# Kernel tuning notes

Hardware: AMD Instinct MI355X
Metric: run time of the kernel (lower is better)

Reference implementation:

```python
import jax, jax.numpy as jnp
import numpy as np

STATE_DIM = 32
ACTION_DIM = 8
LATENT_DIM = 64
HIDDEN = 128
X_DIM = ACTION_DIM + 1  # t channel + actions
B = 4096
L = 128
N_SUB = 2  # fixed RK4 substeps per knot interval


def natural_cubic_coeffs(x):
    """Natural cubic spline on unit-spaced knots 0..L-1 (matches torchcde's
    implicit arange grid). x: [B, L, C]. Returns per-interval coeffs b, c, d
    ([B, L-1, C]) s.t. X(i+u) = x_i + b u + c u^2 + d u^3."""
    Bb, Ln, C = x.shape
    n = Ln - 2
    # tridiagonal system for interior second derivatives (natural BC: m0=mL-1=0)
    M = 4.0 * jnp.eye(n, dtype=x.dtype) + jnp.eye(n, k=1, dtype=x.dtype) + jnp.eye(n, k=-1, dtype=x.dtype)
    rhs = 6.0 * (x[:, 2:] - 2.0 * x[:, 1:-1] + x[:, :-2])  # [B, n, C]
    m_in = jnp.linalg.solve(M, rhs.transpose(1, 0, 2).reshape(n, -1))  # [n, B*C]
    m_in = m_in.reshape(n, Bb, C).transpose(1, 0, 2)
    zpad = jnp.zeros((Bb, 1, C), x.dtype)
    m = jnp.concatenate([zpad, m_in, zpad], axis=1)  # [B, L, C]
    b = (x[:, 1:] - x[:, :-1]) - (2.0 * m[:, :-1] + m[:, 1:]) / 6.0
    c = m[:, :-1] / 2.0
    d = (m[:, 1:] - m[:, :-1]) / 6.0
    return b, c, d


def setup_inputs() -> dict:
    key = jax.random.key(0)
    ks = jax.random.split(key, 8)
    s = jax.random.normal(ks[0], (B, L, STATE_DIM), dtype=jnp.float32)
    a = jax.random.normal(ks[1], (B, L, ACTION_DIM), dtype=jnp.float32)
    t = jnp.broadcast_to(jnp.arange(L, dtype=jnp.float32), (B, L)) + jnp.zeros((B, L), jnp.float32)

    def lin(k, fi, fo, scale=1.0):
        return (jax.random.normal(k, (fi, fo), dtype=jnp.float32) * (scale / np.sqrt(fi))).astype(jnp.float32)

    enc_W = lin(ks[2], STATE_DIM + ACTION_DIM + 1, LATENT_DIM)
    enc_b = jnp.zeros((LATENT_DIM,), jnp.float32)
    f_W1 = lin(ks[3], LATENT_DIM, HIDDEN, 0.5)
    f_b1 = jnp.zeros((HIDDEN,), jnp.float32)
    f_W2 = lin(ks[4], HIDDEN, LATENT_DIM * X_DIM, 0.1)  # small scale keeps the CDE stable over 127 time units
    f_b2 = jnp.zeros((LATENT_DIM * X_DIM,), jnp.float32)
    dec_W = lin(ks[5], LATENT_DIM, STATE_DIM)
    dec_b = jnp.zeros((STATE_DIM,), jnp.float32)
    return dict(s=s, a=a, t=t, enc_W=enc_W, enc_b=enc_b, f_W1=f_W1, f_b1=f_b1,
                f_W2=f_W2, f_b2=f_b2, dec_W=dec_W, dec_b=dec_b)


def reference(s, a, t, enc_W, enc_b, f_W1, f_b1, f_W2, f_b2, dec_W, dec_b):
    # control path X = [t, a] : [B, L, X_DIM]
    x = jnp.concatenate([t[..., None], a], axis=-1)
    cb, cc, cd = natural_cubic_coeffs(x)  # each [B, L-1, X_DIM]

    z0 = jnp.concatenate([s[:, 0], a[:, 0], t[:, 0:1]], axis=-1) @ enc_W + enc_b  # [B, latent]

    def vf(z):  # f(z): [B, latent] -> [B, latent, X_DIM]
        h = jax.nn.relu(z @ f_W1 + f_b1)
        return (h @ f_W2 + f_b2).reshape(-1, LATENT_DIM, X_DIM)

    hstep = 1.0 / N_SUB

    def interval(z, coef):
        bi, ci, di = coef  # [B, X_DIM] each, current interval spline coeffs

        def dzdu(z, u):
            dX = bi + 2.0 * ci * u + 3.0 * di * (u * u)  # dX/dt on this interval
            return jnp.einsum('blx,bx->bl', vf(z), dX)

        for k in range(N_SUB):  # small fixed unroll, not a data-dim loop
            u = k * hstep
            k1 = dzdu(z, u)
            k2 = dzdu(z + 0.5 * hstep * k1, u + 0.5 * hstep)
            k3 = dzdu(z + 0.5 * hstep * k2, u + 0.5 * hstep)
            k4 = dzdu(z + hstep * k3, u + hstep)
            z = z + (hstep / 6.0) * (k1 + 2.0 * k2 + 2.0 * k3 + k4)
        return z, z

    coefs = (cb.transpose(1, 0, 2), cc.transpose(1, 0, 2), cd.transpose(1, 0, 2))  # [L-1, B, X_DIM]
    _, zs = jax.lax.scan(interval, z0, coefs)  # zs: [L-1, B, latent]
    z = jnp.concatenate([z0[None], zs], axis=0).transpose(1, 0, 2)  # [B, L, latent]
    return z @ dec_W + dec_b  # [B, L, state_dim]
```

## Files before the change

kernel.cpp:

```cpp
#include <hip/hip_runtime.h>

#define Bsz 4096
#define Lsz 128
#define NI  127
#define SD  32
#define AD  8
#define LAT 64
#define HID 128
#define BT  16
#define THR 1024

typedef float f32x2 __attribute__((ext_vector_type(2)));
typedef float f32x4 __attribute__((ext_vector_type(4)));

__global__ __launch_bounds__(256) void repack_w2(const float* __restrict__ W2,
                                                 float* __restrict__ W2p8,
                                                 float* __restrict__ W2c0){
  int idx = blockIdx.x*256 + threadIdx.x;
  if (idx < HID*LAT*8){
    int x = idx & 7; int jl = idx >> 3; int l = jl & 63; int j = jl >> 6;
    W2p8[idx] = W2[(j*LAT + l)*9 + x + 1];
  } else if (idx < HID*LAT*9){
    int jl = idx - HID*LAT*8;
    W2c0[jl] = W2[(size_t)jl*9];
  }
}

__global__ __launch_bounds__(256) void spline_kernel(const float* __restrict__ a,
                                                     float* __restrict__ m_ws){
  __shared__ float cp_s[126];
  if (threadIdx.x == 0){
    float c = 0.25f; cp_s[0] = c;
    for (int i=1;i<126;i++){ c = 1.0f/(4.0f - c); cp_s[i] = c; }
  }
  __syncthreads();
  int tid = blockIdx.x*256 + threadIdx.x;
  int b = tid >> 3, c8 = tid & 7;
  float dp[126];
  const float* ab = a + (size_t)b*Lsz*AD + c8;
  float x0 = ab[0];
  float x1 = ab[AD];
  for (int i=0;i<126;i++){
    float x2 = ab[(size_t)(i+2)*AD];
    float rhs = 6.0f*(x2 - 2.0f*x1 + x0);
    dp[i] = (i==0)? rhs*0.25f : (rhs - dp[i-1])*cp_s[i];
    x0 = x1; x1 = x2;
  }
  m_ws[tid] = 0.0f;
  m_ws[((size_t)127*Bsz)*8 + tid] = 0.0f;
  float mn = 0.0f;
  for (int k=125;k>=0;k--){
    mn = dp[k] - cp_s[k]*mn;
    m_ws[((size_t)(k+1)*Bsz)*8 + tid] = mn;
  }
}

#define DPP_XOR1(v) __int_as_float(__builtin_amdgcn_mov_dpp(__float_as_int(v), 0xB1, 0xF, 0xF, true))
#define DPP_XOR2(v) __int_as_float(__builtin_amdgcn_mov_dpp(__float_as_int(v), 0x4E, 0xF, 0xF, true))
#define SWZ_XOR4(v) __int_as_float(__builtin_amdgcn_ds_swizzle(__float_as_int(v), 0x101F))
#define SWZ_XOR8(v) __int_as_float(__builtin_amdgcn_ds_swizzle(__float_as_int(v), 0x201F))

#define PK_MUL_BCLO(d, w, x) asm("v_pk_mul_f32 %0, %1, %2 op_sel:[0,0] op_sel_hi:[0,1]" : "=v"(d) : "v"(w), "v"(x))
#define PK_FMA_BCLO(acc, w, x) asm("v_pk_fma_f32 %0, %1, %2, %0 op_sel:[0,0,0] op_sel_hi:[0,1,1]" : "+v"(acc) : "v"(w), "v"(x))
#define PK_FMA_BCHI(acc, w, x) asm("v_pk_fma_f32 %0, %1, %2, %0 op_sel:[1,0,0] op_sel_hi:[1,1,1]" : "+v"(acc) : "v"(w), "v"(x))
#define PK_FMA(acc, a, b)      asm("v_pk_fma_f32 %0, %1, %2, %0" : "+v"(acc) : "v"(a), "v"(b))
#define PK_ADD(d, a, b)        asm("v_pk_add_f32 %0, %1, %2" : "=v"(d) : "v"(a), "v"(b))

#define LO2(v4) __builtin_shufflevector(v4, v4, 0, 1)
#define HI2(v4) __builtin_shufflevector(v4, v4, 2, 3)

#define HPROW 324
#define DXROW 20

__attribute__((amdgpu_waves_per_eu(4,4)))
__global__ __launch_bounds__(THR) void cde_integrate(
    const float* __restrict__ s, const float* __restrict__ a, const float* __restrict__ t,
    const float* __restrict__ encW, const float* __restrict__ encb,
    const float* __restrict__ W1, const float* __restrict__ b1,
    const float* __restrict__ b2, const float* __restrict__ decW, const float* __restrict__ decb,
    const float* __restrict__ W2p8, const float* __restrict__ W2c0, const float* __restrict__ m_ws,
    float* __restrict__ out)
{
  __shared__ float W1t[HID][LAT+4];
  __shared__ float hp[8*HPROW];
  __shared__ float zs[BT][LAT+4];
  __shared__ float dXp[5*160];
  __shared__ float dWs[LAT][SD];
  __shared__ float b1s[HID];
  __shared__ float b2s[LAT][12];
  __shared__ float dbs[SD];

  const int tid = threadIdx.x;
  const int b0 = blockIdx.x * BT;

  for (int i=tid;i<HID*LAT;i+=THR){ int j = i & (HID-1); int k = i >> 7; W1t[j][k] = W1[k*HID+j]; }
  for (int i=tid;i<LAT*SD;i+=THR)  ((float*)dWs)[i] = decW[i];
  if (tid < HID) b1s[tid] = b1[tid];
  for (int i=tid;i<LAT*12;i+=THR){ int l=i/12, x=i%12; b2s[l][x] = (x<9)? b2[l*9+x] : 0.f; }
  if (tid < SD) dbs[tid] = decb[tid];

  const int ol = tid >> 4;
  const int jg = tid & 15;

  f32x2 wpk[8][4]; f32x2 wc0pk[4];
  {
    #pragma unroll
    for (int jj=0;jj<8;jj++){
      const f32x2* p2 = (const f32x2*)&W2p8[((size_t)(jg*8+jj)*LAT + ol)*8];
      wpk[jj][0]=p2[0]; wpk[jj][1]=p2[1]; wpk[jj][2]=p2[2]; wpk[jj][3]=p2[3];
    }
    #pragma unroll
    for (int q=0;q<4;q++){
      wc0pk[q].x = W2c0[(jg*8+2*q)*LAT + ol];
      wc0pk[q].y = W2c0[(jg*8+2*q+1)*LAT + ol];
    }
  }
  const f32x2 one11 = {1.0f, 1.0f};

  {
    const int bb = tid >> 6;
    const int li = tid & 63;
    const float* sb = s + (size_t)(b0+bb)*Lsz*SD;
    const float* ab = a + (size_t)(b0+bb)*Lsz*AD;
    const float tv = t[(size_t)(b0+bb)*Lsz];
    float acc = encb[li];
    #pragma unroll
    for (int k=0;k<SD;k++) acc = fmaf(sb[k], encW[k*LAT+li], acc);
    #pragma unroll
    for (int k=0;k<AD;k++) acc = fmaf(ab[k], encW[(SD+k)*LAT+li], acc);
    acc = fmaf(tv, encW[(SD+AD)*LAT+li], acc);
    zs[bb][li] = acc;
  }
  __syncthreads();

  if (tid < BT*SD){
    const int bb = tid >> 5; const int o = tid & 31;
    float acc = dbs[o];
    #pragma unroll 8
    for (int k=0;k<LAT;k++) acc = fmaf(zs[bb][k], dWs[k][o], acc);
    out[((size_t)(b0+bb)*Lsz + 0)*SD + o] = acc;
  }

  float zb = zs[jg][ol];
  float ka = 0.f;

  const int hwaddr = (jg>>1)*HPROW + (ol>>2)*20 + ((2*ol)&7)*2 + (jg&1);

  for (int iv=0; iv<NI; iv++){
    if (tid < 5*BT*8){
      int ui = tid >> 7; int r = tid & 127; int bb = r >> 3; int x8 = r & 7;
      float u = 0.25f*(float)ui;
      int gb = b0+bb;
      float m0 = m_ws[((size_t)iv    *Bsz + gb)*8 + x8];
      float m1 = m_ws[((size_t)(iv+1)*Bsz + gb)*8 + x8];
      float xd = a[((size_t)gb*Lsz + iv+1)*AD + x8] - a[((size_t)gb*Lsz + iv)*AD + x8];
      float cb = xd - (2.f*m0 + m1)*(1.f/6.f);
      float cc = 0.5f*m0;
      float cd = (m1 - m0)*(1.f/6.f);
      dXp[ui*160 + (bb>>1)*DXROW + x8*2 + (bb&1)] = cb + (2.f*cc)*u + (3.f*cd)*(u*u);
    }

    for (int st=0; st<8; st++){
      const int ui = (st+1)>>1;
      const int mode = st & 3;
      __syncthreads();

      {
        const int j0 = 2*ol;
        float acc0 = b1s[j0], acc1 = b1s[j0+1];
        const float4* z4 = (const float4*)&zs[jg][0];
        const float4* w0 = (const float4*)&W1t[j0][0];
        const float4* w1 = (const float4*)&W1t[j0+1][0];
        #pragma unroll
        for (int k4=0;k4<LAT/4;k4++){
          float4 zv = z4[k4]; float4 u0 = w0[k4]; float4 u1 = w1[k4];
          acc0 = fmaf(zv.x,u0.x,acc0); acc0 = fmaf(zv.y,u0.y,acc0);
          acc0 = fmaf(zv.z,u0.z,acc0); acc0 = fmaf(zv.w,u0.w,acc0);
          acc1 = fmaf(zv.x,u1.x,acc1); acc1 = fmaf(zv.y,u1.y,acc1);
          acc1 = fmaf(zv.z,u1.z,acc1); acc1 = fmaf(zv.w,u1.w,acc1);
        }
        hp[hwaddr]   = fmaxf(acc0, 0.f);
        hp[hwaddr+2] = fmaxf(acc1, 0.f);
      }
      __syncthreads();

      f32x2 tot0, tot1;
      #pragma unroll
      for (int bbat=0; bbat<2; bbat++){
        f32x2 dzp[4];
        #pragma unroll
        for (int i=0;i<4;i++){ dzp[i].x = 0.f; dzp[i].y = 0.f; }
        #pragma unroll
        for (int pi=0; pi<4; pi++){
          const int p = bbat*4 + pi;
          const f32x4* dxq = (const f32x4*)&dXp[ui*160 + p*DXROW];
          const f32x4* hq  = (const f32x4*)&hp[p*HPROW + jg*20];
          f32x4 d0=dxq[0], d1=dxq[1], d2=dxq[2], d3=dxq[3];
          f32x4 g0=hq[0],  g1=hq[1],  g2=hq[2],  g3=hq[3];
          f32x2 dx2[8] = {LO2(d0),HI2(d0),LO2(d1),HI2(d1),LO2(d2),HI2(d2),LO2(d3),HI2(d3)};
          f32x2 hh [8] = {LO2(g0),HI2(g0),LO2(g1),HI2(g1),LO2(g2),HI2(g2),LO2(g3),HI2(g3)};
          #pragma unroll
          for (int jj=0;jj<8;jj++){
            f32x2 wd;
            PK_MUL_BCLO(wd, wpk[jj][0], dx2[0]);
            PK_FMA_BCHI(wd, wpk[jj][0], dx2[1]);
            PK_FMA_BCLO(wd, wpk[jj][1], dx2[2]);
            PK_FMA_BCHI(wd, wpk[jj][1], dx2[3]);
            PK_FMA_BCLO(wd, wpk[jj][2], dx2[4]);
            PK_FMA_BCHI(wd, wpk[jj][2], dx2[5]);
            PK_FMA_BCLO(wd, wpk[jj][3], dx2[6]);
            PK_FMA_BCHI(wd, wpk[jj][3], dx2[7]);
            if ((jj&1)==0){ PK_FMA_BCLO(wd, wc0pk[jj>>1], one11); }
            else          { PK_FMA_BCHI(wd, wc0pk[jj>>1], one11); }
            PK_FMA(dzp[pi], hh[jj], wd);
          }
        }
        const bool g1 = (jg>>1)&1;
        f32x2 nd[2];
        #pragma unroll
        for (int i=0;i<2;i++){
          f32x2 lo = dzp[2*i], hi = dzp[2*i+1];
          f32x2 send = g1 ? lo : hi;
          f32x2 recv; recv.x = DPP_XOR2(send.x); recv.y = DPP_XOR2(send.y);
          f32x2 keep = g1 ? hi : lo;
          PK_ADD(nd[i], keep, recv);
        }
        const bool g2 = (jg>>2)&1;
        f32x2 md;
        {
          f32x2 lo = nd[0], hi = nd[1];
          f32x2 send = g2 ? lo : hi;
          f32x2 recv; recv.x = SWZ_XOR4(send.x); recv.y = SWZ_XOR4(send.y);
          f32x2 keep = g2 ? hi : lo;
          PK_ADD(md, keep, recv);
        }
        f32x2 r8; r8.x = SWZ_XOR8(md.x); r8.y = SWZ_XOR8(md.y);
        f32x2 totv; PK_ADD(totv, md, r8);
        if (bbat==0) tot0 = totv; else tot1 = totv;
      }
      f32x2 sel = (jg&8) ? tot1 : tot0;
      float own = (jg&1) ? sel.y : sel.x;
      float oth = (jg&1) ? sel.x : sel.y;
      float dzm = own + DPP_XOR1(oth);

      {
        const f32x4* dxb = (const f32x4*)&dXp[ui*160 + (jg>>1)*DXROW];
        f32x4 q0=dxb[0], q1=dxb[1], q2=dxb[2], q3=dxb[3];
        const bool hi = (jg&1);
        float d0 = hi? q0.y:q0.x, d1 = hi? q0.w:q0.z;
        float d2 = hi? q1.y:q1.x, d3 = hi? q1.w:q1.z;
        float d4 = hi? q2.y:q2.x, d5 = hi? q2.w:q2.z;
        float d6 = hi? q3.y:q3.x, d7 = hi? q3.w:q3.z;
        const float4 ba = *(const float4*)&b2s[ol][0];
        const float4 bb4 = *(const float4*)&b2s[ol][4];
        float bias = fmaf(ba.y,d0, fmaf(ba.z,d1, fmaf(ba.w,d2, fmaf(bb4.x,d3,
                     fmaf(bb4.y,d4, fmaf(bb4.z,d5, fmaf(bb4.w,d6, fmaf(b2s[ol][8],d7, ba.x))))))));
        dzm += bias;
      }

      if (mode == 0){        ka = dzm;
        zs[jg][ol] = zb + 0.25f*dzm;
      } else if (mode == 1){ ka = fmaf(2.f, dzm, ka);
        zs[jg][ol] = zb + 0.25f*dzm;
      } else if (mode == 2){ ka = fmaf(2.f, dzm, ka);
        zs[jg][ol] = zb + 0.5f*dzm;
      } else {               ka += dzm;
        zb = fmaf(0.5f/6.f, ka, zb);
        zs[jg][ol] = zb;
      }
    }

    __syncthreads();
    if (tid < BT*SD){
      const int bb = tid >> 5; const int o = tid & 31;
      float acc = dbs[o];
      #pragma unroll 8
      for (int k=0;k<LAT;k++) acc = fmaf(zs[bb][k], dWs[k][o], acc);
      out[((size_t)(b0+bb)*Lsz + (iv+1))*SD + o] = acc;
    }
  }
}

extern "C" void kernel_launch(void* const* d_in, const int* in_sizes, int n_in,
                              void* d_out, int out_size, void* d_ws, size_t ws_size,
                              hipStream_t stream){
  const float* s    = (const float*)d_in[0];
  const float* a    = (const float*)d_in[1];
  const float* t    = (const float*)d_in[2];
  const float* encW = (const float*)d_in[3];
  const float* encb = (const float*)d_in[4];
  const float* W1   = (const float*)d_in[5];
  const float* b1   = (const float*)d_in[6];
  const float* W2   = (const float*)d_in[7];
  const float* b2   = (const float*)d_in[8];
  const float* decW = (const float*)d_in[9];
  const float* decb = (const float*)d_in[10];
  float* out = (float*)d_out;
  float* ws  = (float*)d_ws;
  float* W2p8 = ws;
  float* W2c0 = ws + HID*LAT*8;
  float* m_ws = ws + HID*LAT*9;

  hipLaunchKernelGGL(repack_w2, dim3((HID*LAT*9+255)/256), dim3(256), 0, stream, W2, W2p8, W2c0);
  hipLaunchKernelGGL(spline_kernel, dim3(Bsz*8/256), dim3(256), 0, stream, a, m_ws);
  hipLaunchKernelGGL(cde_integrate, dim3(Bsz/BT), dim3(THR), 0, stream,
                     s,a,t,encW,encb,W1,b1,b2,decW,decb,W2p8,W2c0,m_ws,out);
}
```

Before: 8.841 ms.

## Halve block threads, give each thread 16 hidden units and two batch rows

Cuts the block to 512 threads with 2 waves per EU. Each thread now keeps twice as many W2 weights in registers (16 hidden units) and computes two batch elements packed with v_pk instructions. The layer-1 matmul, the bias and the state update are all done with packed FMAs on interleaved z pairs, and the b1/b2 biases move from LDS into registers. The cross-lane reduction shrinks to an 8-lane xor tree. This aims to cut LDS traffic and reduction overhead per FLOP, at the cost of much higher register pressure and lower occupancy.

```diff
diff --git a/kernel.cpp b/kernel.cpp
--- a/kernel.cpp
+++ b/kernel.cpp
@@ -8,7 +8,7 @@
 #define LAT 64
 #define HID 128
 #define BT  16
-#define THR 1024
+#define THR 512
 
 typedef float f32x2 __attribute__((ext_vector_type(2)));
 typedef float f32x4 __attribute__((ext_vector_type(4)));
@@ -58,9 +58,9 @@
 #define DPP_XOR1(v) __int_as_float(__builtin_amdgcn_mov_dpp(__float_as_int(v), 0xB1, 0xF, 0xF, true))
 #define DPP_XOR2(v) __int_as_float(__builtin_amdgcn_mov_dpp(__float_as_int(v), 0x4E, 0xF, 0xF, true))
 #define SWZ_XOR4(v) __int_as_float(__builtin_amdgcn_ds_swizzle(__float_as_int(v), 0x101F))
-#define SWZ_XOR8(v) __int_as_float(__builtin_amdgcn_ds_swizzle(__float_as_int(v), 0x201F))
 
 #define PK_MUL_BCLO(d, w, x) asm("v_pk_mul_f32 %0, %1, %2 op_sel:[0,0] op_sel_hi:[0,1]" : "=v"(d) : "v"(w), "v"(x))
+#define PK_MUL_BCHI(d, w, x) asm("v_pk_mul_f32 %0, %1, %2 op_sel:[1,0] op_sel_hi:[1,1]" : "=v"(d) : "v"(w), "v"(x))
 #define PK_FMA_BCLO(acc, w, x) asm("v_pk_fma_f32 %0, %1, %2, %0 op_sel:[0,0,0] op_sel_hi:[0,1,1]" : "+v"(acc) : "v"(w), "v"(x))
 #define PK_FMA_BCHI(acc, w, x) asm("v_pk_fma_f32 %0, %1, %2, %0 op_sel:[1,0,0] op_sel_hi:[1,1,1]" : "+v"(acc) : "v"(w), "v"(x))
 #define PK_FMA(acc, a, b)      asm("v_pk_fma_f32 %0, %1, %2, %0" : "+v"(acc) : "v"(a), "v"(b))
@@ -69,10 +69,7 @@
 #define LO2(v4) __builtin_shufflevector(v4, v4, 0, 1)
 #define HI2(v4) __builtin_shufflevector(v4, v4, 2, 3)
 
-#define HPROW 324
-#define DXROW 20
-
-__attribute__((amdgpu_waves_per_eu(4,4)))
+__attribute__((amdgpu_waves_per_eu(2,2)))
 __global__ __launch_bounds__(THR) void cde_integrate(
     const float* __restrict__ s, const float* __restrict__ a, const float* __restrict__ t,
     const float* __restrict__ encW, const float* __restrict__ encb,
@@ -82,73 +79,85 @@
     float* __restrict__ out)
 {
   __shared__ float W1t[HID][LAT+4];
-  __shared__ float hp[8*HPROW];
-  __shared__ float zs[BT][LAT+4];
-  __shared__ float dXp[5*160];
+  __shared__ float hp[8][292];
+  __shared__ float zp[8][132];
+  __shared__ float dXp[5][8][20];
   __shared__ float dWs[LAT][SD];
-  __shared__ float b1s[HID];
-  __shared__ float b2s[LAT][12];
   __shared__ float dbs[SD];
 
   const int tid = threadIdx.x;
   const int b0 = blockIdx.x * BT;
+  const int ol = tid >> 3;
+  const int jg = tid & 7;
 
   for (int i=tid;i<HID*LAT;i+=THR){ int j = i & (HID-1); int k = i >> 7; W1t[j][k] = W1[k*HID+j]; }
   for (int i=tid;i<LAT*SD;i+=THR)  ((float*)dWs)[i] = decW[i];
-  if (tid < HID) b1s[tid] = b1[tid];
-  for (int i=tid;i<LAT*12;i+=THR){ int l=i/12, x=i%12; b2s[l][x] = (x<9)? b2[l*9+x] : 0.f; }
   if (tid < SD) dbs[tid] = decb[tid];
 
-  const int ol = tid >> 4;
-  const int jg = tid & 15;
-
-  f32x2 wpk[8][4]; f32x2 wc0pk[4];
+  f32x2 wpk[16][4]; f32x2 wc0pk[8];
   {
     #pragma unroll
-    for (int jj=0;jj<8;jj++){
-      const f32x2* p2 = (const f32x2*)&W2p8[((size_t)(jg*8+jj)*LAT + ol)*8];
+    for (int jj=0;jj<16;jj++){
+      const f32x2* p2 = (const f32x2*)&W2p8[((size_t)(jg*16+jj)*LAT + ol)*8];
       wpk[jj][0]=p2[0]; wpk[jj][1]=p2[1]; wpk[jj][2]=p2[2]; wpk[jj][3]=p2[3];
     }
     #pragma unroll
-    for (int q=0;q<4;q++){
-      wc0pk[q].x = W2c0[(jg*8+2*q)*LAT + ol];
-      wc0pk[q].y = W2c0[(jg*8+2*q+1)*LAT + ol];
-    }
-  }
-  const f32x2 one11 = {1.0f, 1.0f};
-
+    for (int q=0;q<8;q++){
+      wc0pk[q].x = W2c0[(jg*16+2*q)*LAT + ol];
+      wc0pk[q].y = W2c0[(jg*16+2*q+1)*LAT + ol];
+    }
+    #pragma unroll
+    for (int jj=0;jj<16;jj++){
+      asm volatile("" : "+v"(wpk[jj][0]), "+v"(wpk[jj][1]), "+v"(wpk[jj][2]), "+v"(wpk[jj][3]));
+    }
+  }
+  f32x2 b2p[4]; f32x2 b2c0v; f32x2 b1pair; f32x2 one11; one11.x = 1.f; one11.y = 1.f;
   {
-    const int bb = tid >> 6;
+    const float* bp = b2 + ol*9;
+    b2c0v.x = bp[0]; b2c0v.y = 0.f;
+    b2p[0].x = bp[1]; b2p[0].y = bp[2];
+    b2p[1].x = bp[3]; b2p[1].y = bp[4];
+    b2p[2].x = bp[5]; b2p[2].y = bp[6];
+    b2p[3].x = bp[7]; b2p[3].y = bp[8];
+    b1pair.x = b1[2*ol]; b1pair.y = b1[2*ol+1];
+  }
+
+  {
+    const int bb8 = tid >> 6;
     const int li = tid & 63;
-    const float* sb = s + (size_t)(b0+bb)*Lsz*SD;
-    const float* ab = a + (size_t)(b0+bb)*Lsz*AD;
-    const float tv = t[(size_t)(b0+bb)*Lsz];
-    float acc = encb[li];
     #pragma unroll
-    for (int k=0;k<SD;k++) acc = fmaf(sb[k], encW[k*LAT+li], acc);
-    #pragma unroll
-    for (int k=0;k<AD;k++) acc = fmaf(ab[k], encW[(SD+k)*LAT+li], acc);
-    acc = fmaf(tv, encW[(SD+AD)*LAT+li], acc);
-    zs[bb][li] = acc;
+    for (int h=0; h<2; h++){
+      const int b = bb8 + 8*h;
+      const float* sb = s + (size_t)(b0+b)*Lsz*SD;
+      const float* ab = a + (size_t)(b0+b)*Lsz*AD;
+      const float tv = t[(size_t)(b0+b)*Lsz];
+      float acc = encb[li];
+      #pragma unroll
+      for (int k=0;k<SD;k++) acc = fmaf(sb[k], encW[k*LAT+li], acc);
+      #pragma unroll
+      for (int k=0;k<AD;k++) acc = fmaf(ab[k], encW[(SD+k)*LAT+li], acc);
+      acc = fmaf(tv, encW[(SD+AD)*LAT+li], acc);
+      zp[b>>1][li*2 + (b&1)] = acc;
+    }
   }
   __syncthreads();
 
-  if (tid < BT*SD){
-    const int bb = tid >> 5; const int o = tid & 31;
+  {
+    const int bb = tid >> 5; const int o = tid & 31; const int c = bb & 1;
+    const float* zrow = &zp[bb>>1][0];
     float acc = dbs[o];
-    #pragma unroll 8
-    for (int k=0;k<LAT;k++) acc = fmaf(zs[bb][k], dWs[k][o], acc);
+    #pragma unroll 16
+    for (int k=0;k<LAT;k++) acc = fmaf(zrow[2*k+c], dWs[k][o], acc);
     out[((size_t)(b0+bb)*Lsz + 0)*SD + o] = acc;
   }
 
-  float zb = zs[jg][ol];
-  float ka = 0.f;
-
-  const int hwaddr = (jg>>1)*HPROW + (ol>>2)*20 + ((2*ol)&7)*2 + (jg&1);
-
+  float zb0, zb1, ka0 = 0.f, ka1 = 0.f;
+  { f32x2 zr = *(const f32x2*)&zp[jg][2*ol]; zb0 = zr.x; zb1 = zr.y; }
+
+  #pragma unroll 1
   for (int iv=0; iv<NI; iv++){
-    if (tid < 5*BT*8){
-      int ui = tid >> 7; int r = tid & 127; int bb = r >> 3; int x8 = r & 7;
+    for (int idx=tid; idx<5*BT*8; idx+=THR){
+      int ui = idx >> 7; int r = idx & 127; int bb = r >> 3; int x8 = r & 7;
       float u = 0.25f*(float)ui;
       int gb = b0+bb;
       float m0 = m_ws[((size_t)iv    *Bsz + gb)*8 + x8];
@@ -157,9 +166,10 @@
       float cb = xd - (2.f*m0 + m1)*(1.f/6.f);
       float cc = 0.5f*m0;
       float cd = (m1 - m0)*(1.f/6.f);
-      dXp[ui*160 + (bb>>1)*DXROW + x8*2 + (bb&1)] = cb + (2.f*cc)*u + (3.f*cd)*(u*u);
-    }
-
+      dXp[ui][bb>>1][x8*2 + (bb&1)] = cb + (2.f*cc)*u + (3.f*cd)*(u*u);
+    }
+
+    #pragma unroll 1
     for (int st=0; st<8; st++){
       const int ui = (st+1)>>1;
       const int mode = st & 3;
@@ -167,115 +177,133 @@
 
       {
         const int j0 = 2*ol;
-        float acc0 = b1s[j0], acc1 = b1s[j0+1];
-        const float4* z4 = (const float4*)&zs[jg][0];
-        const float4* w0 = (const float4*)&W1t[j0][0];
-        const float4* w1 = (const float4*)&W1t[j0+1][0];
+        f32x2 acc0, acc1;
+        PK_MUL_BCLO(acc0, b1pair, one11);
+        PK_MUL_BCHI(acc1, b1pair, one11);
+        const f32x4* zrow = (const f32x4*)&zp[jg][0];
+        const f32x4* w0r = (const f32x4*)&W1t[j0][0];
+        const f32x4* w1r = (const f32x4*)&W1t[j0+1][0];
         #pragma unroll
-        for (int k4=0;k4<LAT/4;k4++){
-          float4 zv = z4[k4]; float4 u0 = w0[k4]; float4 u1 = w1[k4];
-          acc0 = fmaf(zv.x,u0.x,acc0); acc0 = fmaf(zv.y,u0.y,acc0);
-          acc0 = fmaf(zv.z,u0.z,acc0); acc0 = fmaf(zv.w,u0.w,acc0);
-          acc1 = fmaf(zv.x,u1.x,acc1); acc1 = fmaf(zv.y,u1.y,acc1);
-          acc1 = fmaf(zv.z,u1.z,acc1); acc1 = fmaf(zv.w,u1.w,acc1);
+        for (int k16=0;k16<16;k16++){
+          f32x4 zqA = zrow[2*k16], zqB = zrow[2*k16+1];
+          f32x4 w0q = w0r[k16], w1q = w1r[k16];
+          f32x2 w0l = LO2(w0q), w0h = HI2(w0q), w1l = LO2(w1q), w1h = HI2(w1q);
+          f32x2 zA0 = LO2(zqA), zA1 = HI2(zqA), zB0 = LO2(zqB), zB1 = HI2(zqB);
+          PK_FMA_BCLO(acc0, w0l, zA0); PK_FMA_BCHI(acc0, w0l, zA1);
+          PK_FMA_BCLO(acc0, w0h, zB0); PK_FMA_BCHI(acc0, w0h, zB1);
+          PK_FMA_BCLO(acc1, w1l, zA0); PK_FMA_BCHI(acc1, w1l, zA1);
+          PK_FMA_BCLO(acc1, w1h, zB0); PK_FMA_BCHI(acc1, w1h, zB1);
         }
-        hp[hwaddr]   = fmaxf(acc0, 0.f);
-        hp[hwaddr+2] = fmaxf(acc1, 0.f);
+        f32x4 hv;
+        hv.x = fmaxf(acc0.x, 0.f); hv.y = fmaxf(acc0.y, 0.f);
+        hv.z = fmaxf(acc1.x, 0.f); hv.w = fmaxf(acc1.y, 0.f);
+        *(f32x4*)&hp[jg][(ol>>3)*36 + (ol&7)*4] = hv;
       }
       __syncthreads();
 
-      f32x2 tot0, tot1;
-      #pragma unroll
-      for (int bbat=0; bbat<2; bbat++){
-        f32x2 dzp[4];
+      f32x2 dz[8];
+      #pragma unroll
+      for (int p=0;p<8;p++){
+        const f32x4* dxr = (const f32x4*)&dXp[ui][p][0];
+        f32x4 d0=dxr[0], d1=dxr[1], d2=dxr[2], d3=dxr[3];
+        f32x2 dx2[8] = {LO2(d0),HI2(d0),LO2(d1),HI2(d1),LO2(d2),HI2(d2),LO2(d3),HI2(d3)};
+        const f32x4* hr = (const f32x4*)&hp[p][jg*36];
+        f32x2 acc; acc.x = 0.f; acc.y = 0.f;
         #pragma unroll
-        for (int i=0;i<4;i++){ dzp[i].x = 0.f; dzp[i].y = 0.f; }
-        #pragma unroll
-        for (int pi=0; pi<4; pi++){
-          const int p = bbat*4 + pi;
-          const f32x4* dxq = (const f32x4*)&dXp[ui*160 + p*DXROW];
-          const f32x4* hq  = (const f32x4*)&hp[p*HPROW + jg*20];
-          f32x4 d0=dxq[0], d1=dxq[1], d2=dxq[2], d3=dxq[3];
-          f32x4 g0=hq[0],  g1=hq[1],  g2=hq[2],  g3=hq[3];
-          f32x2 dx2[8] = {LO2(d0),HI2(d0),LO2(d1),HI2(d1),LO2(d2),HI2(d2),LO2(d3),HI2(d3)};
-          f32x2 hh [8] = {LO2(g0),HI2(g0),LO2(g1),HI2(g1),LO2(g2),HI2(g2),LO2(g3),HI2(g3)};
-          #pragma unroll
-          for (int jj=0;jj<8;jj++){
+        for (int jj2=0;jj2<8;jj2++){
+          f32x4 hq = hr[jj2];
+          f32x2 hl = LO2(hq), hh = HI2(hq);
+          {
             f32x2 wd;
-            PK_MUL_BCLO(wd, wpk[jj][0], dx2[0]);
-            PK_FMA_BCHI(wd, wpk[jj][0], dx2[1]);
-            PK_FMA_BCLO(wd, wpk[jj][1], dx2[2]);
-            PK_FMA_BCHI(wd, wpk[jj][1], dx2[3]);
-            PK_FMA_BCLO(wd, wpk[jj][2], dx2[4]);
-            PK_FMA_BCHI(wd, wpk[jj][2], dx2[5]);
-            PK_FMA_BCLO(wd, wpk[jj][3], dx2[6]);
-            PK_FMA_BCHI(wd, wpk[jj][3], dx2[7]);
-            if ((jj&1)==0){ PK_FMA_BCLO(wd, wc0pk[jj>>1], one11); }
-            else          { PK_FMA_BCHI(wd, wc0pk[jj>>1], one11); }
-            PK_FMA(dzp[pi], hh[jj], wd);
+            PK_MUL_BCLO(wd, wpk[2*jj2][0], dx2[0]); PK_FMA_BCHI(wd, wpk[2*jj2][0], dx2[1]);
+            PK_FMA_BCLO(wd, wpk[2*jj2][1], dx2[2]); PK_FMA_BCHI(wd, wpk[2*jj2][1], dx2[3]);
+            PK_FMA_BCLO(wd, wpk[2*jj2][2], dx2[4]); PK_FMA_BCHI(wd, wpk[2*jj2][2], dx2[5]);
+            PK_FMA_BCLO(wd, wpk[2*jj2][3], dx2[6]); PK_FMA_BCHI(wd, wpk[2*jj2][3], dx2[7]);
+            PK_FMA_BCLO(wd, wc0pk[jj2], one11);
+            PK_FMA(acc, hl, wd);
+          }
+          {
+            f32x2 wd;
+            PK_MUL_BCLO(wd, wpk[2*jj2+1][0], dx2[0]); PK_FMA_BCHI(wd, wpk[2*jj2+1][0], dx2[1]);
+            PK_FMA_BCLO(wd, wpk[2*jj2+1][1], dx2[2]); PK_FMA_BCHI(wd, wpk[2*jj2+1][1], dx2[3]);
+            PK_FMA_BCLO(wd, wpk[2*jj2+1][2], dx2[4]); PK_FMA_BCHI(wd, wpk[2*jj2+1][2], dx2[5]);
+            PK_FMA_BCLO(wd, wpk[2*jj2+1][3], dx2[6]); PK_FMA_BCHI(wd, wpk[2*jj2+1][3], dx2[7]);
+            PK_FMA_BCHI(wd, wc0pk[jj2], one11);
+            PK_FMA(acc, hh, wd);
           }
         }
-        const bool g1 = (jg>>1)&1;
-        f32x2 nd[2];
-        #pragma unroll
-        for (int i=0;i<2;i++){
-          f32x2 lo = dzp[2*i], hi = dzp[2*i+1];
-          f32x2 send = g1 ? lo : hi;
-          f32x2 recv; recv.x = DPP_XOR2(send.x); recv.y = DPP_XOR2(send.y);
-          f32x2 keep = g1 ? hi : lo;
-          PK_ADD(nd[i], keep, recv);
-        }
-        const bool g2 = (jg>>2)&1;
-        f32x2 md;
-        {
-          f32x2 lo = nd[0], hi = nd[1];
-          f32x2 send = g2 ? lo : hi;
-          f32x2 recv; recv.x = SWZ_XOR4(send.x); recv.y = SWZ_XOR4(send.y);
-          f32x2 keep = g2 ? hi : lo;
-          PK_ADD(md, keep, recv);
-        }
-        f32x2 r8; r8.x = SWZ_XOR8(md.x); r8.y = SWZ_XOR8(md.y);
-        f32x2 totv; PK_ADD(totv, md, r8);
-        if (bbat==0) tot0 = totv; else tot1 = totv;
-      }
-      f32x2 sel = (jg&8) ? tot1 : tot0;
-      float own = (jg&1) ? sel.y : sel.x;
-      float oth = (jg&1) ? sel.x : sel.y;
-      float dzm = own + DPP_XOR1(oth);
-
+        dz[p] = acc;
+      }
+
+      const bool g1 = jg & 1;
+      f32x2 n4[4];
+      #pragma unroll
+      for (int i=0;i<4;i++){
+        f32x2 lo = dz[2*i], hi = dz[2*i+1];
+        f32x2 send = g1 ? lo : hi;
+        f32x2 recv; recv.x = DPP_XOR1(send.x); recv.y = DPP_XOR1(send.y);
+        f32x2 keep = g1 ? hi : lo;
+        PK_ADD(n4[i], keep, recv);
+      }
+      const bool g2 = jg & 2;
+      f32x2 n2[2];
+      #pragma unroll
+      for (int i=0;i<2;i++){
+        f32x2 lo = n4[2*i], hi = n4[2*i+1];
+        f32x2 send = g2 ? lo : hi;
+        f32x2 recv; recv.x = DPP_XOR2(send.x); recv.y = DPP_XOR2(send.y);
+        f32x2 keep = g2 ? hi : lo;
+        PK_ADD(n2[i], keep, recv);
+      }
+      const bool g4 = jg & 4;
+      f32x2 res;
       {
-        const f32x4* dxb = (const f32x4*)&dXp[ui*160 + (jg>>1)*DXROW];
-        f32x4 q0=dxb[0], q1=dxb[1], q2=dxb[2], q3=dxb[3];
-        const bool hi = (jg&1);
-        float d0 = hi? q0.y:q0.x, d1 = hi? q0.w:q0.z;
-        float d2 = hi? q1.y:q1.x, d3 = hi? q1.w:q1.z;
-        float d4 = hi? q2.y:q2.x, d5 = hi? q2.w:q2.z;
-        float d6 = hi? q3.y:q3.x, d7 = hi? q3.w:q3.z;
-        const float4 ba = *(const float4*)&b2s[ol][0];
-        const float4 bb4 = *(const float4*)&b2s[ol][4];
-        float bias = fmaf(ba.y,d0, fmaf(ba.z,d1, fmaf(ba.w,d2, fmaf(bb4.x,d3,
-                     fmaf(bb4.y,d4, fmaf(bb4.z,d5, fmaf(bb4.w,d6, fmaf(b2s[ol][8],d7, ba.x))))))));
-        dzm += bias;
-      }
-
-      if (mode == 0){        ka = dzm;
-        zs[jg][ol] = zb + 0.25f*dzm;
-      } else if (mode == 1){ ka = fmaf(2.f, dzm, ka);
-        zs[jg][ol] = zb + 0.25f*dzm;
-      } else if (mode == 2){ ka = fmaf(2.f, dzm, ka);
-        zs[jg][ol] = zb + 0.5f*dzm;
-      } else {               ka += dzm;
-        zb = fmaf(0.5f/6.f, ka, zb);
-        zs[jg][ol] = zb;
-      }
+        f32x2 lo = n2[0], hi = n2[1];
+        f32x2 send = g4 ? lo : hi;
+        f32x2 recv; recv.x = SWZ_XOR4(send.x); recv.y = SWZ_XOR4(send.y);
+        f32x2 keep = g4 ? hi : lo;
+        PK_ADD(res, keep, recv);
+      }
+
+      f32x2 bias2;
+      {
+        const f32x4* dxb = (const f32x4*)&dXp[ui][jg][0];
+        f32x4 e0=dxb[0], e1=dxb[1], e2=dxb[2], e3=dxb[3];
+        PK_MUL_BCLO(bias2, b2c0v, one11);
+        PK_FMA_BCLO(bias2, b2p[0], LO2(e0)); PK_FMA_BCHI(bias2, b2p[0], HI2(e0));
+        PK_FMA_BCLO(bias2, b2p[1], LO2(e1)); PK_FMA_BCHI(bias2, b2p[1], HI2(e1));
+        PK_FMA_BCLO(bias2, b2p[2], LO2(e2)); PK_FMA_BCHI(bias2, b2p[2], HI2(e2));
+        PK_FMA_BCLO(bias2, b2p[3], LO2(e3)); PK_FMA_BCHI(bias2, b2p[3], HI2(e3));
+      }
+      f32x2 dzm2; PK_ADD(dzm2, res, bias2);
+      const float dz0 = dzm2.x, dz1 = dzm2.y;
+
+      float zn0, zn1;
+      if (mode == 0){
+        ka0 = dz0; ka1 = dz1;
+        zn0 = fmaf(0.25f, dz0, zb0); zn1 = fmaf(0.25f, dz1, zb1);
+      } else if (mode == 1){
+        ka0 = fmaf(2.f, dz0, ka0); ka1 = fmaf(2.f, dz1, ka1);
+        zn0 = fmaf(0.25f, dz0, zb0); zn1 = fmaf(0.25f, dz1, zb1);
+      } else if (mode == 2){
+        ka0 = fmaf(2.f, dz0, ka0); ka1 = fmaf(2.f, dz1, ka1);
+        zn0 = fmaf(0.5f, dz0, zb0); zn1 = fmaf(0.5f, dz1, zb1);
+      } else {
+        ka0 += dz0; ka1 += dz1;
+        zb0 = fmaf(0.5f/6.f, ka0, zb0); zb1 = fmaf(0.5f/6.f, ka1, zb1);
+        zn0 = zb0; zn1 = zb1;
+      }
+      f32x2 zw; zw.x = zn0; zw.y = zn1;
+      *(f32x2*)&zp[jg][2*ol] = zw;
     }
 
     __syncthreads();
-    if (tid < BT*SD){
-      const int bb = tid >> 5; const int o = tid & 31;
+    {
+      const int bb = tid >> 5; const int o = tid & 31; const int c = bb & 1;
+      const float* zrow = &zp[bb>>1][0];
       float acc = dbs[o];
-      #pragma unroll 8
-      for (int k=0;k<LAT;k++) acc = fmaf(zs[bb][k], dWs[k][o], acc);
+      #pragma unroll 16
+      for (int k=0;k<LAT;k++) acc = fmaf(zrow[2*k+c], dWs[k][o], acc);
       out[((size_t)(b0+bb)*Lsz + (iv+1))*SD + o] = acc;
     }
   }
```

Measured after the change: 8.486 ms. 1.04x faster.
